# Optimization experiments

Measured on AMD Instinct MI355X. Metric: run time of the kernel, lower is better.

The kernel has to match this reference:

```python
import jax, jax.numpy as jnp
import numpy as np

ORIG_IN = 4096
ORIG_OUT = 4096
ACTIVE = 2048
RANK = 16
SCALING = 32.0 / 16.0  # lora_alpha / r


def setup_inputs() -> dict:
    key = jax.random.key(0)
    ks = jax.random.split(key, 7)
    x = jax.random.normal(ks[0], (2, 4096, ORIG_IN), dtype=jnp.float32)
    W_base = jax.random.normal(ks[1], (ACTIVE, ACTIVE), dtype=jnp.float32) * 0.02
    b_base = jax.random.normal(ks[2], (ACTIVE,), dtype=jnp.float32) * 0.02
    lora_A = jax.random.normal(ks[3], (RANK, ACTIVE), dtype=jnp.float32) * 0.02
    # lora_B is zero-initialized in the module, but use small random values so
    # the LoRA path contributes non-trivially to the baseline computation.
    lora_B = jax.random.normal(ks[4], (ACTIVE, RANK), dtype=jnp.float32) * 0.02
    # sorted unique index subsets (pruning masks)
    in_indices = jnp.sort(jax.random.permutation(ks[5], ORIG_IN)[:ACTIVE]).astype(jnp.int32)
    out_indices = jnp.sort(jax.random.permutation(ks[6], ORIG_OUT)[:ACTIVE]).astype(jnp.int32)
    return {
        "x": x, "W_base": W_base, "b_base": b_base,
        "lora_A": lora_A, "lora_B": lora_B,
        "in_indices": in_indices, "out_indices": out_indices,
    }


def reference(x, W_base, b_base, lora_A, lora_B, in_indices, out_indices):
    batch_dims = x.shape[:-1]
    x_flat = x.reshape(-1, ORIG_IN)            # [N, orig_in]
    x_sel = x_flat[:, in_indices]              # gather -> [N, active]
    # LoRA path: (x @ A^T) @ B^T * scaling  (dropout = identity, eval mode)
    lora_out = jnp.einsum('na,ra->nr', x_sel, lora_A)
    lora_out = jnp.einsum('nr,or->no', lora_out, lora_B) * SCALING
    # Base pruned linear
    base_out = jnp.einsum('na,oa->no', x_sel, W_base) + b_base
    combined = base_out + lora_out             # [N, active]
    # Scatter into zero-initialized full output
    out_flat = jnp.zeros((x_flat.shape[0], ORIG_OUT), dtype=combined.dtype)
    out_flat = out_flat.at[:, out_indices].set(combined)
    return out_flat.reshape(batch_dims + (ORIG_OUT,))
```

## Files before the change

kernel.cpp:

```cpp
#include <hip/hip_runtime.h>
#include <hip/hip_bf16.h>
#include <stdint.h>

#define M_DIM 8192
#define K_DIM 2048
#define N_DIM 2048
#define IN_DIM 4096
#define OUT_DIM 4096
#define SCALING 2.0f

typedef __attribute__((ext_vector_type(8))) short bf16x8_t;
typedef __attribute__((ext_vector_type(4))) float f32x4_t;

__device__ __forceinline__ void load_lds16(const void* gptr, void* lptr) {
    __builtin_amdgcn_global_load_lds(
        (const __attribute__((address_space(1))) uint32_t*)(uintptr_t)gptr,
        (__attribute__((address_space(3))) uint32_t*)(uintptr_t)lptr,
        16, 0, 0);
}

__global__ void fold_w_kernel(const float* __restrict__ Wb,
                              const float* __restrict__ lA,
                              const float* __restrict__ lB,
                              __hip_bfloat16* __restrict__ We) {
    const int k = blockIdx.x * 256 + threadIdx.x;
    const int o = blockIdx.y;
    float acc = Wb[(size_t)o * K_DIM + k];
    #pragma unroll
    for (int r = 0; r < 16; ++r)
        acc += SCALING * lB[o * 16 + r] * lA[r * K_DIM + k];
    We[(size_t)o * K_DIM + k] = __float2bfloat16(acc);
}

__global__ void __launch_bounds__(256)
gather_cast_kernel(const float* __restrict__ x,
                   const int* __restrict__ idx,
                   __hip_bfloat16* __restrict__ xs) {
    __shared__ float row[IN_DIM];
    const int n = blockIdx.x;
    const float* xrow = x + (size_t)n * IN_DIM;
    #pragma unroll
    for (int i = 0; i < 4; ++i) {
        const int c = (i * 256 + threadIdx.x) * 4;
        *(float4*)&row[c] = *(const float4*)&xrow[c];
    }
    __syncthreads();
    const int c0 = threadIdx.x * 8;
    int4 i0 = *(const int4*)(idx + c0);
    int4 i1 = *(const int4*)(idx + c0 + 4);
    union { bf16x8_t v; __hip_bfloat16 h[8]; } u;
    u.h[0] = __float2bfloat16(row[i0.x]);
    u.h[1] = __float2bfloat16(row[i0.y]);
    u.h[2] = __float2bfloat16(row[i0.z]);
    u.h[3] = __float2bfloat16(row[i0.w]);
    u.h[4] = __float2bfloat16(row[i1.x]);
    u.h[5] = __float2bfloat16(row[i1.y]);
    u.h[6] = __float2bfloat16(row[i1.z]);
    u.h[7] = __float2bfloat16(row[i1.w]);
    *(bf16x8_t*)(xs + (size_t)n * K_DIM + c0) = u.v;
}

__global__ void build_inv_kernel(const int* __restrict__ oidx,
                                 int* __restrict__ inv) {
    const int c = blockIdx.x * 256 + threadIdx.x;
    int lo = 0, hi = N_DIM;
    while (lo < hi) {
        const int mid = (lo + hi) >> 1;
        if (oidx[mid] < c) lo = mid + 1; else hi = mid;
    }
    inv[c] = (lo < N_DIM && oidx[lo] == c) ? lo : -1;
}

template <bool COMPACT>
__global__ void __launch_bounds__(256, 2)
gemm_kernel(const __hip_bfloat16* __restrict__ A,
            const __hip_bfloat16* __restrict__ B,
            const float* __restrict__ bias,
            const int* __restrict__ oidx,
            float* __restrict__ out,
            __hip_bfloat16* __restrict__ Cc)
{
    __shared__ __hip_bfloat16 As[128 * 64];
    __shared__ __hip_bfloat16 Bs[128 * 64];

    const int tid  = threadIdx.x;
    const int wave = tid >> 6;
    const int lane = tid & 63;
    const int m0 = blockIdx.y * 128;
    const int n0 = blockIdx.x * 128;

    const int wm = (wave >> 1) * 64;
    const int wn = (wave & 1) * 64;

    const int srow  = tid >> 3;
    const int sslot = tid & 7;

    const int r15 = lane & 15;
    const int qd  = lane >> 4;

    f32x4_t acc[4][4] = {};

    for (int k0 = 0; k0 < K_DIM; k0 += 64) {
        #pragma unroll
        for (int it = 0; it < 4; ++it) {
            const int row = it * 32 + srow;
            const int q = sslot ^ (row & 7);
            const __hip_bfloat16* ga = A + (size_t)(m0 + row) * K_DIM + k0 + q * 8;
            const __hip_bfloat16* gb = B + (size_t)(n0 + row) * K_DIM + k0 + q * 8;
            load_lds16(ga, (void*)&As[(it * 32 + wave * 8) * 64]);
            load_lds16(gb, (void*)&Bs[(it * 32 + wave * 8) * 64]);
        }
        __syncthreads();

        #pragma unroll
        for (int s = 0; s < 2; ++s) {
            bf16x8_t af[4], bfr[4];
            #pragma unroll
            for (int i = 0; i < 4; ++i) {
                const int rowa = wm + i * 16 + r15;
                const int pa = (s * 4 + qd) ^ (rowa & 7);
                af[i] = *(const bf16x8_t*)&As[rowa * 64 + pa * 8];
                const int rowb = wn + i * 16 + r15;
                const int pb = (s * 4 + qd) ^ (rowb & 7);
                bfr[i] = *(const bf16x8_t*)&Bs[rowb * 64 + pb * 8];
            }
            #pragma unroll
            for (int i = 0; i < 4; ++i)
                #pragma unroll
                for (int j = 0; j < 4; ++j)
                    acc[i][j] = __builtin_amdgcn_mfma_f32_16x16x32_bf16(
                        af[i], bfr[j], acc[i][j], 0, 0, 0);
        }
        __syncthreads();
    }

    #pragma unroll
    for (int j = 0; j < 4; ++j) {
        const int gn = n0 + wn + j * 16 + r15;
        const float bv = bias[gn];
        if (COMPACT) {
            #pragma unroll
            for (int i = 0; i < 4; ++i) {
                const int gm = m0 + wm + i * 16 + qd * 4;
                #pragma unroll
                for (int r = 0; r < 4; ++r)
                    Cc[(size_t)(gm + r) * N_DIM + gn] =
                        __float2bfloat16(acc[i][j][r] + bv);
            }
        } else {
            const int oc = oidx[gn];
            #pragma unroll
            for (int i = 0; i < 4; ++i) {
                const int gm = m0 + wm + i * 16 + qd * 4;
                #pragma unroll
                for (int r = 0; r < 4; ++r)
                    out[(size_t)(gm + r) * OUT_DIM + oc] = acc[i][j][r] + bv;
            }
        }
    }
}

__global__ void __launch_bounds__(256)
scatter_out_kernel(const __hip_bfloat16* __restrict__ C,
                   const int* __restrict__ inv,
                   float* __restrict__ out) {
    const int row = blockIdx.y;
    const int c0 = (blockIdx.x * 256 + threadIdx.x) * 4;
    const __hip_bfloat16* crow = C + (size_t)row * N_DIM;
    const int4 iv = *(const int4*)(inv + c0);
    float4 v;
    v.x = (iv.x >= 0) ? __bfloat162float(crow[iv.x]) : 0.0f;
    v.y = (iv.y >= 0) ? __bfloat162float(crow[iv.y]) : 0.0f;
    v.z = (iv.z >= 0) ? __bfloat162float(crow[iv.z]) : 0.0f;
    v.w = (iv.w >= 0) ? __bfloat162float(crow[iv.w]) : 0.0f;
    *(float4*)(out + (size_t)row * OUT_DIM + c0) = v;
}

extern "C" void kernel_launch(void* const* d_in, const int* in_sizes, int n_in,
                              void* d_out, int out_size, void* d_ws, size_t ws_size,
                              hipStream_t stream) {
    const float* x      = (const float*)d_in[0];
    const float* W_base = (const float*)d_in[1];
    const float* b_base = (const float*)d_in[2];
    const float* lora_A = (const float*)d_in[3];
    const float* lora_B = (const float*)d_in[4];
    const int* in_idx   = (const int*)d_in[5];
    const int* out_idx  = (const int*)d_in[6];
    float* out = (float*)d_out;

    const size_t sz_xs = (size_t)M_DIM * K_DIM * 2;
    const size_t sz_We = (size_t)N_DIM * K_DIM * 2;
    const size_t sz_C  = (size_t)M_DIM * N_DIM * 2;
    const size_t sz_inv = (size_t)OUT_DIM * 4;

    __hip_bfloat16* xs = (__hip_bfloat16*)d_ws;
    __hip_bfloat16* We = (__hip_bfloat16*)((char*)d_ws + sz_xs);
    __hip_bfloat16* Cc = (__hip_bfloat16*)((char*)d_ws + sz_xs + sz_We);
    int* inv           = (int*)((char*)d_ws + sz_xs + sz_We + sz_C);

    fold_w_kernel<<<dim3(K_DIM / 256, N_DIM), 256, 0, stream>>>(W_base, lora_A, lora_B, We);
    gather_cast_kernel<<<M_DIM, 256, 0, stream>>>(x, in_idx, xs);

    if (ws_size >= sz_xs + sz_We + sz_C + sz_inv) {
        build_inv_kernel<<<OUT_DIM / 256, 256, 0, stream>>>(out_idx, inv);
        gemm_kernel<true><<<dim3(N_DIM / 128, M_DIM / 128), 256, 0, stream>>>(
            xs, We, b_base, out_idx, out, Cc);
        scatter_out_kernel<<<dim3(OUT_DIM / (256 * 4), M_DIM), 256, 0, stream>>>(
            Cc, inv, out);
    } else {
        hipMemsetAsync(d_out, 0, (size_t)M_DIM * OUT_DIM * sizeof(float), stream);
        gemm_kernel<false><<<dim3(N_DIM / 128, M_DIM / 128), 256, 0, stream>>>(
            xs, We, b_base, out_idx, out, Cc);
    }
}
```

Measured before the change: 344.8 us.

## Replace compact GEMM with 256x256 tile kernel using 4-stage LDS pipeline

Adds a 512-thread GEMM kernel with 256x256 output tiles and a 4-buffer ring of 32-wide K slices in LDS. Global-to-LDS loads for future stages are issued while MFMAs run on the current stage, and waits use partial vmcnt plus barriers, with setprio around the MFMA blocks. The aim is to hide memory latency and raise arithmetic intensity compared with the 128x128 single-buffered kernel. The cost is heavy register use for 32 accumulators per thread, a 128 KB LDS footprint, and only 256 blocks across the device.

```diff
diff --git a/kernel.cpp b/kernel.cpp
--- a/kernel.cpp
+++ b/kernel.cpp
@@ -71,6 +71,119 @@
     inv[c] = (lo < N_DIM && oidx[lo] == c) ? lo : -1;
 }
 
+__device__ __forceinline__ bf16x8_t frag_ld(const __hip_bfloat16* buf, int row, int qd) {
+    const int p = qd ^ ((row >> 1) & 3);
+    return *(const bf16x8_t*)(buf + row * 32 + p * 8);
+}
+
+__device__ __forceinline__ void stage_call(const __hip_bfloat16* __restrict__ G,
+                                           int grow0,
+                                           __hip_bfloat16* region,
+                                           int lrow0,
+                                           int w, int l, int k0) {
+    const int rr   = w * 16 + (l >> 2);
+    const int lrow = lrow0 + rr;
+    const int kc   = (l & 3) ^ ((lrow >> 1) & 3);
+    load_lds16(G + (size_t)(grow0 + rr) * K_DIM + k0 + kc * 8,
+               (void*)(region + (size_t)(lrow0 + w * 16) * 32));
+}
+
+__global__ void __launch_bounds__(512, 2)
+gemm256_kernel(const __hip_bfloat16* __restrict__ A,
+               const __hip_bfloat16* __restrict__ B,
+               const float* __restrict__ bias,
+               __hip_bfloat16* __restrict__ Cc)
+{
+    __shared__ __hip_bfloat16 lds[4][2][256 * 32];
+
+    const int tid = threadIdx.x;
+    const int w   = tid >> 6;
+    const int l   = tid & 63;
+    const int r15 = l & 15;
+    const int qd  = l >> 4;
+    const int wm  = w >> 2;
+    const int wn  = w & 3;
+    const int m0  = blockIdx.y * 256;
+    const int n0  = blockIdx.x * 256;
+
+    f32x4_t acc[8][4] = {};
+
+    #pragma unroll
+    for (int t = 0; t < 3; ++t) {
+        const int k0 = t * 32;
+        stage_call(A, m0,       lds[t][0], 0,   w, l, k0);
+        stage_call(A, m0 + 128, lds[t][0], 128, w, l, k0);
+        stage_call(B, n0,       lds[t][1], 0,   w, l, k0);
+        stage_call(B, n0 + 128, lds[t][1], 128, w, l, k0);
+    }
+    asm volatile("s_waitcnt vmcnt(8)" ::: "memory");
+    __builtin_amdgcn_sched_barrier(0);
+    __builtin_amdgcn_s_barrier();
+
+    for (int tt = 0; tt < 64; tt += 4) {
+        #pragma unroll
+        for (int c = 0; c < 4; ++c) {
+            const int bs  = c;
+            const int bt  = (c + 3) & 3;
+            const int k0s = ((tt + c + 3) & 63) * 32;
+            const __hip_bfloat16* Ab = lds[bs][0];
+            const __hip_bfloat16* Bb = lds[bs][1];
+
+            bf16x8_t af[4], bfr[4];
+            #pragma unroll
+            for (int i = 0; i < 4; ++i)
+                af[i] = frag_ld(Ab, wm * 128 + i * 16 + r15, qd);
+            #pragma unroll
+            for (int j = 0; j < 4; ++j)
+                bfr[j] = frag_ld(Bb, wn * 64 + j * 16 + r15, qd);
+            stage_call(A, m0,       lds[bt][0], 0,   w, l, k0s);
+            stage_call(A, m0 + 128, lds[bt][0], 128, w, l, k0s);
+            __builtin_amdgcn_s_barrier();
+            __builtin_amdgcn_s_setprio(1);
+            #pragma unroll
+            for (int i = 0; i < 4; ++i)
+                #pragma unroll
+                for (int j = 0; j < 4; ++j)
+                    acc[i][j] = __builtin_amdgcn_mfma_f32_16x16x32_bf16(
+                        af[i], bfr[j], acc[i][j], 0, 0, 0);
+            __builtin_amdgcn_s_setprio(0);
+
+            #pragma unroll
+            for (int i = 0; i < 4; ++i)
+                af[i] = frag_ld(Ab, wm * 128 + (4 + i) * 16 + r15, qd);
+            stage_call(B, n0,       lds[bt][1], 0,   w, l, k0s);
+            stage_call(B, n0 + 128, lds[bt][1], 128, w, l, k0s);
+            __builtin_amdgcn_s_barrier();
+            __builtin_amdgcn_s_setprio(1);
+            #pragma unroll
+            for (int i = 0; i < 4; ++i)
+                #pragma unroll
+                for (int j = 0; j < 4; ++j)
+                    acc[4 + i][j] = __builtin_amdgcn_mfma_f32_16x16x32_bf16(
+                        af[i], bfr[j], acc[4 + i][j], 0, 0, 0);
+            __builtin_amdgcn_s_setprio(0);
+            asm volatile("s_waitcnt vmcnt(8)" ::: "memory");
+            __builtin_amdgcn_sched_barrier(0);
+            __builtin_amdgcn_s_barrier();
+        }
+    }
+    asm volatile("s_waitcnt vmcnt(0)" ::: "memory");
+
+    #pragma unroll
+    for (int j = 0; j < 4; ++j) {
+        const int gn = n0 + wn * 64 + j * 16 + r15;
+        const float bv = bias[gn];
+        #pragma unroll
+        for (int i = 0; i < 8; ++i) {
+            const int gm = m0 + wm * 128 + i * 16 + qd * 4;
+            #pragma unroll
+            for (int r = 0; r < 4; ++r)
+                Cc[(size_t)(gm + r) * N_DIM + gn] =
+                    __float2bfloat16(acc[i][j][r] + bv);
+        }
+    }
+}
+
 template <bool COMPACT>
 __global__ void __launch_bounds__(256, 2)
 gemm_kernel(const __hip_bfloat16* __restrict__ A,
@@ -203,8 +316,8 @@
 
     if (ws_size >= sz_xs + sz_We + sz_C + sz_inv) {
         build_inv_kernel<<<OUT_DIM / 256, 256, 0, stream>>>(out_idx, inv);
-        gemm_kernel<true><<<dim3(N_DIM / 128, M_DIM / 128), 256, 0, stream>>>(
-            xs, We, b_base, out_idx, out, Cc);
+        gemm256_kernel<<<dim3(N_DIM / 256, M_DIM / 256), 512, 0, stream>>>(
+            xs, We, b_base, Cc);
         scatter_out_kernel<<<dim3(OUT_DIM / (256 * 4), M_DIM), 256, 0, stream>>>(
             Cc, inv, out);
     } else {
```

Result: no change. 347.4 us (+0.8%).
